# Kernel tuning notes

Hardware: AMD Instinct MI355X
Metric: run time of the kernel (lower is better)

Reference implementation:

```python
import jax, jax.numpy as jnp
import numpy as np

N, NFEAT, NHID, E = 100000, 256, 64, 1600000
EPS = 1e-5
NEG_SLOPE = 0.2


def _glorot(k, shape):
    lim = float(np.sqrt(6.0 / (shape[0] + shape[1])))
    return jax.random.uniform(k, shape, jnp.float32, -lim, lim)


def setup_inputs() -> dict:
    key = jax.random.key(0)
    ks = jax.random.split(key, 24)
    inp = {
        "g": jax.random.normal(ks[0], (N, NFEAT), jnp.float32),           # node features
        "x": jax.random.randint(ks[1], (2, E), 0, N),                      # edge_index [src; dst]
    }
    # estimator GAT params
    inp["est_W"] = _glorot(ks[2], (NFEAT, NHID))
    inp["est_asrc"] = _glorot(ks[3], (NHID, 1))[:, 0]
    inp["est_adst"] = _glorot(ks[4], (NHID, 1))[:, 0]
    inp["est_bias"] = jnp.zeros((NHID,), jnp.float32)
    inp["est_gamma"] = jnp.ones((NHID,), jnp.float32)
    inp["est_beta"] = jnp.zeros((NHID,), jnp.float32)
    inp["est_rmean"] = 0.1 * jax.random.normal(ks[5], (NHID,), jnp.float32)
    inp["est_rvar"] = jax.random.uniform(ks[6], (NHID,), jnp.float32, 0.5, 1.5)
    # GNN GAT params
    inp["gnn_W"] = _glorot(ks[7], (NFEAT, NHID))
    inp["gnn_asrc"] = _glorot(ks[8], (NHID, 1))[:, 0]
    inp["gnn_adst"] = _glorot(ks[9], (NHID, 1))[:, 0]
    inp["gnn_bias"] = jnp.zeros((NHID,), jnp.float32)
    inp["gnn_gamma"] = jnp.ones((NHID,), jnp.float32)
    inp["gnn_beta"] = jnp.zeros((NHID,), jnp.float32)
    inp["gnn_rmean"] = 0.1 * jax.random.normal(ks[10], (NHID,), jnp.float32)
    inp["gnn_rvar"] = jax.random.uniform(ks[11], (NHID,), jnp.float32, 0.5, 1.5)
    # classifier head
    inp["cls_W"] = _glorot(ks[12], (NHID, 1))
    inp["cls_b"] = jnp.zeros((1,), jnp.float32)
    return inp


def _gat(feat, src, dst, W, a_src, a_dst, bias, gamma, beta, rmean, rvar):
    # GATConv (heads=1): linear -> per-edge attention logits -> segment softmax over dst -> weighted scatter
    h = feat @ W                                  # [N, NHID]
    e_src = h @ a_src                             # [N]
    e_dst = h @ a_dst                             # [N]
    e = jax.nn.leaky_relu(e_src[src] + e_dst[dst], NEG_SLOPE)   # [E+N]
    m = jax.ops.segment_max(e, dst, num_segments=N)
    p = jnp.exp(e - m[dst])
    z = jax.ops.segment_sum(p, dst, num_segments=N)
    alpha = p / z[dst]                            # softmax per destination node
    out = jax.ops.segment_sum(h[src] * alpha[:, None], dst, num_segments=N) + bias
    # transition: ReLU -> BatchNorm1d (eval, running stats) -> Dropout (identity in eval)
    out = jnp.maximum(out, 0.0)
    return (out - rmean) * jax.lax.rsqrt(rvar + EPS) * gamma + beta


def reference(g, x, est_W, est_asrc, est_adst, est_bias, est_gamma, est_beta, est_rmean, est_rvar,
              gnn_W, gnn_asrc, gnn_adst, gnn_bias, gnn_gamma, gnn_beta, gnn_rmean, gnn_rvar,
              cls_W, cls_b):
    loop = jnp.arange(N)                          # add_self_loops=True
    src = jnp.concatenate([x[0], loop])
    dst = jnp.concatenate([x[1], loop])
    s = _gat(g, src, dst, est_W, est_asrc, est_adst, est_bias, est_gamma, est_beta, est_rmean, est_rvar)
    z = _gat(g, src, dst, gnn_W, gnn_asrc, gnn_adst, gnn_bias, gnn_gamma, gnn_beta, gnn_rmean, gnn_rvar)
    y = z @ cls_W + cls_b                         # [N, 1]
    return (y, s)
```

## Files before the change

kernel.cpp:

```cpp
#include <hip/hip_runtime.h>
#include <math.h>
#include <float.h>

#define NFEAT 256
#define NHID 64
#define BN_EPS 1e-5f

typedef float f32x4 __attribute__((ext_vector_type(4)));
typedef short s16x8 __attribute__((ext_vector_type(8)));

__device__ __forceinline__ float lrelu(float x) { return x >= 0.f ? x : 0.2f * x; }
__device__ __forceinline__ unsigned short f2bf(float f) {
    unsigned int u = __float_as_uint(f);
    return (unsigned short)((u + 0x7fffu + ((u >> 16) & 1u)) >> 16);
}
__device__ __forceinline__ float bf_lo(unsigned int v) { return __uint_as_float(v << 16); }
__device__ __forceinline__ float bf_hi(unsigned int v) { return __uint_as_float(v & 0xffff0000u); }

__global__ void prep_w_k(const float* __restrict__ We, const float* __restrict__ Wg,
                         unsigned short* __restrict__ Wt, int* __restrict__ bcnt) {
    if (blockIdx.x == 0) bcnt[threadIdx.x] = 0;
    int tid = blockIdx.x * 256 + threadIdx.x;
    int ks  = tid >> 12;
    int col = (tid >> 5) & 127;
    int kk  = tid & 31;
    int k   = ks * 32 + kk;
    float v = (col < 64) ? We[k * 64 + col] : Wg[k * 64 + (col - 64)];
    size_t byte = (size_t)ks * 10240 + col * 80 + (kk >> 3) * 16 + (kk & 7) * 2;
    Wt[byte >> 1] = f2bf(v);
}

__global__ void bucket_hist_k(const int* __restrict__ x, int E, int* __restrict__ bcnt) {
    __shared__ int lh[256];
    int tid = threadIdx.x;
    lh[tid] = 0;
    __syncthreads();
    int base = (blockIdx.x * 256 + tid) * 32;
#pragma unroll
    for (int c = 0; c < 8; ++c) {
        int b4 = base + c * 4;
        if (b4 + 4 <= E) {
            int4 d = *(const int4*)(x + E + b4);
            atomicAdd(&lh[d.x >> 9], 1); atomicAdd(&lh[d.y >> 9], 1);
            atomicAdd(&lh[d.z >> 9], 1); atomicAdd(&lh[d.w >> 9], 1);
        } else {
            for (int k = 0; k < 4; ++k)
                if (b4 + k < E) atomicAdd(&lh[x[E + b4 + k] >> 9], 1);
        }
    }
    __syncthreads();
    if (lh[tid] > 0) atomicAdd(&bcnt[tid], lh[tid]);
}

__global__ void bucket_scan_k(const int* __restrict__ bcnt, int M, int NBKT,
                              int* __restrict__ bucket_base, int* __restrict__ bcursor,
                              int* __restrict__ csr_base) {
    __shared__ int s_c[2][256], s_t[2][256];
    int tid = threadIdx.x;
    int c = (tid < NBKT) ? bcnt[tid] : 0;
    int n0 = tid << 9;
    int sc = (tid < NBKT) ? min(512, M - n0) : 0;
    int tot = c + sc;
    s_c[0][tid] = c; s_t[0][tid] = tot;
    __syncthreads();
    int cur = 0;
    for (int off = 1; off < 256; off <<= 1) {
        int nc = s_c[cur][tid] + (tid >= off ? s_c[cur][tid - off] : 0);
        int nt = s_t[cur][tid] + (tid >= off ? s_t[cur][tid - off] : 0);
        s_c[cur ^ 1][tid] = nc; s_t[cur ^ 1][tid] = nt;
        __syncthreads();
        cur ^= 1;
    }
    if (tid < NBKT) {
        int eb = s_c[cur][tid] - c;
        bucket_base[tid] = eb;
        bcursor[tid] = eb;
        csr_base[tid] = s_t[cur][tid] - tot;
    }
}

__global__ void bucket_scatter_k(const int* __restrict__ x, int E,
                                 int* __restrict__ bcursor, int* __restrict__ ebuf) {
    __shared__ int lh[256], gb[256];
    int tid = threadIdx.x;
    lh[tid] = 0;
    __syncthreads();
    int base = (blockIdx.x * 256 + tid) * 32;
#pragma unroll
    for (int c = 0; c < 8; ++c) {
        int b4 = base + c * 4;
        if (b4 + 4 <= E) {
            int4 d = *(const int4*)(x + E + b4);
            atomicAdd(&lh[d.x >> 9], 1); atomicAdd(&lh[d.y >> 9], 1);
            atomicAdd(&lh[d.z >> 9], 1); atomicAdd(&lh[d.w >> 9], 1);
        } else {
            for (int k = 0; k < 4; ++k)
                if (b4 + k < E) atomicAdd(&lh[x[E + b4 + k] >> 9], 1);
        }
    }
    __syncthreads();
    if (lh[tid] > 0) gb[tid] = atomicAdd(&bcursor[tid], lh[tid]);
    lh[tid] = 0;
    __syncthreads();
#pragma unroll
    for (int c = 0; c < 8; ++c) {
        int b4 = base + c * 4;
        if (b4 + 4 <= E) {
            int4 s = *(const int4*)(x + b4);
            int4 d = *(const int4*)(x + E + b4);
            int ss[4] = {s.x, s.y, s.z, s.w};
            int dd[4] = {d.x, d.y, d.z, d.w};
#pragma unroll
            for (int k = 0; k < 4; ++k) {
                int bk = dd[k] >> 9;
                int rk = atomicAdd(&lh[bk], 1);
                ebuf[gb[bk] + rk] = ((dd[k] & 511) << 17) | ss[k];
            }
        } else {
            for (int k = 0; k < 4; ++k) {
                int i = b4 + k;
                if (i < E) {
                    int sv = x[i], dv = x[E + i];
                    int bk = dv >> 9;
                    int rk = atomicAdd(&lh[bk], 1);
                    ebuf[gb[bk] + rk] = ((dv & 511) << 17) | sv;
                }
            }
        }
    }
}

__global__ __launch_bounds__(256) void bucket_csr_k(const int* __restrict__ bcnt,
                                                    const int* __restrict__ bucket_base,
                                                    const int* __restrict__ csr_base,
                                                    const int* __restrict__ ebuf, int M,
                                                    int* __restrict__ row_start,
                                                    int* __restrict__ deg,
                                                    int* __restrict__ srcs) {
    int b = blockIdx.x, tid = threadIdx.x;
    int nE = bcnt[b];
    int ebase = bucket_base[b];
    int cbase = csr_base[b];
    int n0 = b << 9;
    int nloc = min(512, M - n0);
    __shared__ int cnt[512], sa[512], sb[512], cur[512];
#pragma unroll
    for (int k = 0; k < 2; ++k) {
        int i = tid + k * 256;
        cnt[i] = (i < nloc) ? 1 : 0;
    }
    __syncthreads();
    for (int j = tid; j < nE; j += 256)
        atomicAdd(&cnt[ebuf[ebase + j] >> 17], 1);
    __syncthreads();
#pragma unroll
    for (int k = 0; k < 2; ++k) { int i = tid + k * 256; sa[i] = cnt[i]; }
    __syncthreads();
    int* a = sa; int* bb = sb;
    for (int off = 1; off < 512; off <<= 1) {
#pragma unroll
        for (int k = 0; k < 2; ++k) {
            int i = tid + k * 256;
            bb[i] = a[i] + (i >= off ? a[i - off] : 0);
        }
        __syncthreads();
        int* t = a; a = bb; bb = t;
    }
#pragma unroll
    for (int k = 0; k < 2; ++k) {
        int i = tid + k * 256;
        int excl = a[i] - cnt[i];
        cur[i] = excl;
        if (i < nloc) {
            row_start[n0 + i] = cbase + excl;
            deg[n0 + i] = cnt[i];
            srcs[cbase + excl] = n0 + i;
            cur[i] = excl + 1;
        }
    }
    __syncthreads();
    for (int j = tid; j < nE; j += 256) {
        int p = ebuf[ebase + j];
        int dl = p >> 17, src = p & 0x1FFFF;
        int pos = atomicAdd(&cur[dl], 1);
        srcs[cbase + pos] = src;
    }
}

__global__ __launch_bounds__(256) void gemm_mfma_k(const float* __restrict__ g,
                                                   const char* __restrict__ Wt,
                                                   unsigned short* __restrict__ hh,
                                                   const float* __restrict__ ase,
                                                   const float* __restrict__ ade,
                                                   const float* __restrict__ asg,
                                                   const float* __restrict__ adg,
                                                   float2* __restrict__ esrc,
                                                   float2* __restrict__ edst, int M) {
    __shared__ __align__(16) char lds[21504];
    char* As = lds;
    char* Bs = lds + 10240;
    float* av = (float*)(lds + 20480);
    const int tid = threadIdx.x;
    const int l = tid & 63;
    const int w = tid >> 6;
    const int row0 = blockIdx.x * 128;

    {
        float v;
        if (tid < 64)       v = ase[tid];
        else if (tid < 128) v = ade[tid - 64];
        else if (tid < 192) v = asg[tid - 128];
        else                v = adg[tid - 192];
        av[tid] = v;
    }

    f32x4 acc[2][8];
#pragma unroll
    for (int r = 0; r < 2; r++)
#pragma unroll
        for (int n = 0; n < 8; n++) acc[r][n] = (f32x4){0.f, 0.f, 0.f, 0.f};

    const int arow = tid >> 1;
    const int ah = tid & 1;
    const int grow = row0 + arow;
    const float* gp = g + (size_t)grow * NFEAT + ah * 16;
    const char* wp = Wt + arow * 80 + ah * 32;

    float4 v0 = make_float4(0.f, 0.f, 0.f, 0.f), v1 = v0, v2 = v0, v3 = v0;
    s16x8 b0, b1;
    if (grow < M) {
        v0 = *(const float4*)(gp + 0);
        v1 = *(const float4*)(gp + 4);
        v2 = *(const float4*)(gp + 8);
        v3 = *(const float4*)(gp + 12);
    }
    b0 = *(const s16x8*)(wp);
    b1 = *(const s16x8*)(wp + 16);

    for (int ks = 0; ks < 8; ++ks) {
        {
            s16x8 c0, c1;
            c0[0]=f2bf(v0.x); c0[1]=f2bf(v0.y); c0[2]=f2bf(v0.z); c0[3]=f2bf(v0.w);
            c0[4]=f2bf(v1.x); c0[5]=f2bf(v1.y); c0[6]=f2bf(v1.z); c0[7]=f2bf(v1.w);
            c1[0]=f2bf(v2.x); c1[1]=f2bf(v2.y); c1[2]=f2bf(v2.z); c1[3]=f2bf(v2.w);
            c1[4]=f2bf(v3.x); c1[5]=f2bf(v3.y); c1[6]=f2bf(v3.z); c1[7]=f2bf(v3.w);
            *(s16x8*)(As + arow * 80 + ah * 32)      = c0;
            *(s16x8*)(As + arow * 80 + ah * 32 + 16) = c1;
            *(s16x8*)(Bs + arow * 80 + ah * 32)      = b0;
            *(s16x8*)(Bs + arow * 80 + ah * 32 + 16) = b1;
        }
        __syncthreads();
        if (ks < 7) {
            const float* gpn = gp + (ks + 1) * 32;
            const char* wpn = wp + (size_t)(ks + 1) * 10240;
            v0 = make_float4(0.f, 0.f, 0.f, 0.f); v1 = v0; v2 = v0; v3 = v0;
            if (grow < M) {
                v0 = *(const float4*)(gpn + 0);
                v1 = *(const float4*)(gpn + 4);
                v2 = *(const float4*)(gpn + 8);
                v3 = *(const float4*)(gpn + 12);
            }
            b0 = *(const s16x8*)(wpn);
            b1 = *(const s16x8*)(wpn + 16);
        }
        s16x8 af[2];
#pragma unroll
        for (int r = 0; r < 2; r++)
            af[r] = *(const s16x8*)(As + (w * 32 + r * 16 + (l & 15)) * 80 + (l >> 4) * 16);
#pragma unroll
        for (int n = 0; n < 8; n++) {
            s16x8 bf = *(const s16x8*)(Bs + (n * 16 + (l & 15)) * 80 + (l >> 4) * 16);
            acc[0][n] = __builtin_amdgcn_mfma_f32_16x16x32_bf16(af[0], bf, acc[0][n], 0, 0, 0);
            acc[1][n] = __builtin_amdgcn_mfma_f32_16x16x32_bf16(af[1], bf, acc[1][n], 0, 0, 0);
        }
        __syncthreads();
    }

    float vs_e[4], vd_e[4], vs_g[4], vd_g[4];
    {
        const int l16 = l & 15;
#pragma unroll
        for (int n = 0; n < 4; ++n) {
            vs_e[n] = av[n * 16 + l16];
            vd_e[n] = av[64 + n * 16 + l16];
            vs_g[n] = av[128 + n * 16 + l16];
            vd_g[n] = av[192 + n * 16 + l16];
        }
    }

    unsigned short* epi = (unsigned short*)lds;
#pragma unroll
    for (int p = 0; p < 2; ++p) {
        {
            float pse[4] = {0,0,0,0}, pde[4] = {0,0,0,0};
            float psg[4] = {0,0,0,0}, pdg[4] = {0,0,0,0};
#pragma unroll
            for (int n = 0; n < 4; ++n)
#pragma unroll
                for (int j = 0; j < 4; ++j) {
                    float he = acc[p][n][j];
                    float hg = acc[p][n + 4][j];
                    pse[j] += he * vs_e[n];
                    pde[j] += he * vd_e[n];
                    psg[j] += hg * vs_g[n];
                    pdg[j] += hg * vd_g[n];
                }
#pragma unroll
            for (int off = 1; off <= 8; off <<= 1) {
#pragma unroll
                for (int j = 0; j < 4; ++j) {
                    pse[j] += __shfl_xor(pse[j], off, 64);
                    pde[j] += __shfl_xor(pde[j], off, 64);
                    psg[j] += __shfl_xor(psg[j], off, 64);
                    pdg[j] += __shfl_xor(pdg[j], off, 64);
                }
            }
            if ((l & 15) == 0) {
#pragma unroll
                for (int j = 0; j < 4; ++j) {
                    int gr = row0 + w * 32 + p * 16 + (l >> 4) * 4 + j;
                    if (gr < M) {
                        esrc[gr] = make_float2(pse[j], psg[j]);
                        edst[gr] = make_float2(pde[j], pdg[j]);
                    }
                }
            }
        }
#pragma unroll
        for (int n = 0; n < 8; n++)
#pragma unroll
            for (int j = 0; j < 4; j++)
                epi[(w * 16 + (l >> 4) * 4 + j) * 128 + n * 16 + (l & 15)] = f2bf(acc[p][n][j]);
        __syncthreads();
        int er = tid >> 2, sgm = tid & 3;
        int grow2 = row0 + 32 * (er >> 4) + 16 * p + (er & 15);
        if (grow2 < M) {
            const s16x8* src = (const s16x8*)(epi + er * 128 + sgm * 32);
            s16x8* dst = (s16x8*)(hh + (size_t)grow2 * 128 + sgm * 32);
#pragma unroll
            for (int q = 0; q < 4; q++) dst[q] = src[q];
        }
        __syncthreads();
    }
}

__global__ void node_acc_k(const int* __restrict__ srcs, const int* __restrict__ row_start,
                           const int* __restrict__ deg,
                           const float2* __restrict__ esrc, const float2* __restrict__ edst,
                           const unsigned short* __restrict__ hh,
                           const float* __restrict__ be, const float* __restrict__ ge,
                           const float* __restrict__ bte, const float* __restrict__ rme,
                           const float* __restrict__ rve,
                           const float* __restrict__ bg, const float* __restrict__ gg,
                           const float* __restrict__ btg, const float* __restrict__ rmg,
                           const float* __restrict__ rvg,
                           const float* __restrict__ clsW, const float* __restrict__ clsb,
                           float* __restrict__ y, float* __restrict__ s_out, int M) {
    int n = blockIdx.x * 4 + (threadIdx.x >> 6);
    int l = threadIdx.x & 63;
    if (n >= M) return;
    int beg = row_start[n];
    int cnt = deg[n];
    int qh = l >> 4;
    int li = l & 15;
    int layer = li >> 3;
    float2 ed = edst[n];
    float edv = layer ? ed.y : ed.x;
    const int* sp = srcs + beg;
    const char* hb = (const char*)hh + (unsigned)li * 16;
    float a0 = 0.f, a1 = 0.f, a2 = 0.f, a3 = 0.f;
    float a4 = 0.f, a5 = 0.f, a6 = 0.f, a7 = 0.f, zacc = 0.f;
    int j = 0;
    for (; j + 16 <= cnt; j += 16) {
        int s0 = sp[j + qh];
        int s1 = sp[j + 4 + qh];
        int s2 = sp[j + 8 + qh];
        int s3 = sp[j + 12 + qh];
        float2 e0 = esrc[s0], e1 = esrc[s1], e2 = esrc[s2], e3 = esrc[s3];
        uint4 h0 = *(const uint4*)(hb + ((size_t)(unsigned)s0 << 8));
        uint4 h1 = *(const uint4*)(hb + ((size_t)(unsigned)s1 << 8));
        uint4 h2 = *(const uint4*)(hb + ((size_t)(unsigned)s2 << 8));
        uint4 h3 = *(const uint4*)(hb + ((size_t)(unsigned)s3 << 8));
        float p0 = __expf(lrelu((layer ? e0.y : e0.x) + edv));
        float p1 = __expf(lrelu((layer ? e1.y : e1.x) + edv));
        float p2 = __expf(lrelu((layer ? e2.y : e2.x) + edv));
        float p3 = __expf(lrelu((layer ? e3.y : e3.x) + edv));
        zacc += (p0 + p1) + (p2 + p3);
        a0 += p0 * bf_lo(h0.x); a1 += p0 * bf_hi(h0.x);
        a2 += p0 * bf_lo(h0.y); a3 += p0 * bf_hi(h0.y);
        a4 += p0 * bf_lo(h0.z); a5 += p0 * bf_hi(h0.z);
        a6 += p0 * bf_lo(h0.w); a7 += p0 * bf_hi(h0.w);
        a0 += p1 * bf_lo(h1.x); a1 += p1 * bf_hi(h1.x);
        a2 += p1 * bf_lo(h1.y); a3 += p1 * bf_hi(h1.y);
        a4 += p1 * bf_lo(h1.z); a5 += p1 * bf_hi(h1.z);
        a6 += p1 * bf_lo(h1.w); a7 += p1 * bf_hi(h1.w);
// ... 67 lines not shown
        o0 = (fmaxf(o0 + bA.x, 0.f) - rmA.x) * rsqrtf(rvA.x + BN_EPS) * gA.x + btA.x;
        o1 = (fmaxf(o1 + bA.y, 0.f) - rmA.y) * rsqrtf(rvA.y + BN_EPS) * gA.y + btA.y;
        o2 = (fmaxf(o2 + bA.z, 0.f) - rmA.z) * rsqrtf(rvA.z + BN_EPS) * gA.z + btA.z;
        o3 = (fmaxf(o3 + bA.w, 0.f) - rmA.w) * rsqrtf(rvA.w + BN_EPS) * gA.w + btA.w;
        o4 = (fmaxf(o4 + bB.x, 0.f) - rmB.x) * rsqrtf(rvB.x + BN_EPS) * gB.x + btB.x;
        o5 = (fmaxf(o5 + bB.y, 0.f) - rmB.y) * rsqrtf(rvB.y + BN_EPS) * gB.y + btB.y;
        o6 = (fmaxf(o6 + bB.z, 0.f) - rmB.z) * rsqrtf(rvB.z + BN_EPS) * gB.z + btB.z;
        o7 = (fmaxf(o7 + bB.w, 0.f) - rmB.w) * rsqrtf(rvB.w + BN_EPS) * gB.w + btB.w;
        if (layer == 0) {
            float4* so = (float4*)(s_out + (size_t)n * 64 + (li & 7) * 8);
            so[0] = make_float4(o0, o1, o2, o3);
            so[1] = make_float4(o4, o5, o6, o7);
        } else {
            float4 wA = ((const float4*)clsW)[cb];
            float4 wB = ((const float4*)clsW)[cb + 1];
            float t = o0 * wA.x + o1 * wA.y + o2 * wA.z + o3 * wA.w
                    + o4 * wB.x + o5 * wB.y + o6 * wB.z + o7 * wB.w;
            t += __shfl_xor(t, 1, 64);
            t += __shfl_xor(t, 2, 64);
            t += __shfl_xor(t, 4, 64);
            if (li == 8) y[n] = t + clsb[0];
        }
    }
}

extern "C" void kernel_launch(void* const* d_in, const int* in_sizes, int n_in,
                              void* d_out, int out_size, void* d_ws, size_t ws_size,
                              hipStream_t stream) {
    const float* g        = (const float*)d_in[0];
    const int*   x        = (const int*)d_in[1];
    const float* est_W    = (const float*)d_in[2];
    const float* est_asrc = (const float*)d_in[3];
    const float* est_adst = (const float*)d_in[4];
    const float* est_bias = (const float*)d_in[5];
    const float* est_gamma= (const float*)d_in[6];
    const float* est_beta = (const float*)d_in[7];
    const float* est_rmean= (const float*)d_in[8];
    const float* est_rvar = (const float*)d_in[9];
    const float* gnn_W    = (const float*)d_in[10];
    const float* gnn_asrc = (const float*)d_in[11];
    const float* gnn_adst = (const float*)d_in[12];
    const float* gnn_bias = (const float*)d_in[13];
    const float* gnn_gamma= (const float*)d_in[14];
    const float* gnn_beta = (const float*)d_in[15];
    const float* gnn_rmean= (const float*)d_in[16];
    const float* gnn_rvar = (const float*)d_in[17];
    const float* cls_W    = (const float*)d_in[18];
    const float* cls_b    = (const float*)d_in[19];

    const int M  = in_sizes[0] / NFEAT;
    const int E  = in_sizes[1] / 2;
    const int Et = E + M;
    const int NBKT = (M + 511) >> 9;

    float* y_out = (float*)d_out;
    float* s_out = y_out + M;

    char* base = (char*)d_ws;
    unsigned short* hh = (unsigned short*)base;
    size_t off = (size_t)M * 128 * 2;
    char* Wt = base + off;                  off += 81920;
    float2* esrc = (float2*)(base + off);   off += (size_t)M * 8;
    float2* edst = (float2*)(base + off);   off += (size_t)M * 8;
    int* deg       = (int*)(base + off);    off += (size_t)M * 4;
    int* row_start = (int*)(base + off);    off += (size_t)M * 4;
    int* srcs      = (int*)(base + off);    off += (size_t)Et * 4;
    int* ebuf      = (int*)(base + off);    off += (size_t)E * 4;
    int* bcnt        = (int*)(base + off);  off += 256 * 4;
    int* bucket_base = (int*)(base + off);  off += 256 * 4;
    int* bcursor     = (int*)(base + off);  off += 256 * 4;
    int* csr_base    = (int*)(base + off);  off += 256 * 4;

    const int EB32 = (E + 8191) / 8192;

    prep_w_k<<<128, 256, 0, stream>>>(est_W, gnn_W, (unsigned short*)Wt, bcnt);
    bucket_hist_k<<<EB32, 256, 0, stream>>>(x, E, bcnt);
    bucket_scan_k<<<1, 256, 0, stream>>>(bcnt, M, NBKT, bucket_base, bcursor, csr_base);
    bucket_scatter_k<<<EB32, 256, 0, stream>>>(x, E, bcursor, ebuf);
    bucket_csr_k<<<NBKT, 256, 0, stream>>>(bcnt, bucket_base, csr_base, ebuf, M,
                                           row_start, deg, srcs);

    gemm_mfma_k<<<(M + 127) / 128, 256, 0, stream>>>(g, Wt, hh,
                                                     est_asrc, est_adst, gnn_asrc, gnn_adst,
                                                     esrc, edst, M);

    node_acc_k<<<(M + 3) / 4, 256, 0, stream>>>(srcs, row_start, deg, esrc, edst, hh,
                                                est_bias, est_gamma, est_beta, est_rmean, est_rvar,
                                                gnn_bias, gnn_gamma, gnn_beta, gnn_rmean, gnn_rvar,
                                                cls_W, cls_b, y_out, s_out, M);
}
```

Measured before the change: 175.3 us.

## Merge preprocessing kernels and co-schedule edge scatter with GEMM blocks

Folds the weight conversion into the histogram kernel. Per-block bucket counts are written out and prefix-scanned in a single block, which makes scatter offsets deterministic and removes the global cursor atomics and the second histogram pass inside the scatter. The edge scatter blocks are then appended to the GEMM grid, so the bucketing work overlaps with the MFMA projection and the launch count drops from seven to five. The cost is a serial per-thread loop over all edge blocks in the single-block scan (about 196 iterations), plus LDS usage shared between two very different block types.

```diff
diff --git a/kernel.cpp b/kernel.cpp
--- a/kernel.cpp
+++ b/kernel.cpp
@@ -17,25 +17,27 @@
 __device__ __forceinline__ float bf_lo(unsigned int v) { return __uint_as_float(v << 16); }
 __device__ __forceinline__ float bf_hi(unsigned int v) { return __uint_as_float(v & 0xffff0000u); }
 
-__global__ void prep_w_k(const float* __restrict__ We, const float* __restrict__ Wg,
-                         unsigned short* __restrict__ Wt, int* __restrict__ bcnt) {
-    if (blockIdx.x == 0) bcnt[threadIdx.x] = 0;
-    int tid = blockIdx.x * 256 + threadIdx.x;
-    int ks  = tid >> 12;
-    int col = (tid >> 5) & 127;
-    int kk  = tid & 31;
-    int k   = ks * 32 + kk;
-    float v = (col < 64) ? We[k * 64 + col] : Wg[k * 64 + (col - 64)];
-    size_t byte = (size_t)ks * 10240 + col * 80 + (kk >> 3) * 16 + (kk & 7) * 2;
-    Wt[byte >> 1] = f2bf(v);
-}
-
-__global__ void bucket_hist_k(const int* __restrict__ x, int E, int* __restrict__ bcnt) {
+__global__ void stage1_k(const float* __restrict__ We, const float* __restrict__ Wg,
+                         unsigned short* __restrict__ Wt,
+                         const int* __restrict__ x, int E,
+                         int* __restrict__ blkcnt) {
+    if (blockIdx.x < 128) {
+        int tid = blockIdx.x * 256 + threadIdx.x;
+        int ks  = tid >> 12;
+        int col = (tid >> 5) & 127;
+        int kk  = tid & 31;
+        int k   = ks * 32 + kk;
+        float v = (col < 64) ? We[k * 64 + col] : Wg[k * 64 + (col - 64)];
+        size_t byte = (size_t)ks * 10240 + col * 80 + (kk >> 3) * 16 + (kk & 7) * 2;
+        Wt[byte >> 1] = f2bf(v);
+        return;
+    }
     __shared__ int lh[256];
+    int blk = blockIdx.x - 128;
     int tid = threadIdx.x;
     lh[tid] = 0;
     __syncthreads();
-    int base = (blockIdx.x * 256 + tid) * 32;
+    int base = (blk * 256 + tid) * 32;
 #pragma unroll
     for (int c = 0; c < 8; ++c) {
         int b4 = base + c * 4;
@@ -49,59 +51,53 @@
         }
     }
     __syncthreads();
-    if (lh[tid] > 0) atomicAdd(&bcnt[tid], lh[tid]);
-}
-
-__global__ void bucket_scan_k(const int* __restrict__ bcnt, int M, int NBKT,
-                              int* __restrict__ bucket_base, int* __restrict__ bcursor,
-                              int* __restrict__ csr_base) {
+    blkcnt[blk * 256 + tid] = lh[tid];
+}
+
+__global__ void scan_k(int* __restrict__ blkcnt, int NEB, int M, int NBKT,
+                       int* __restrict__ blkbase,
+                       int* __restrict__ bcnt, int* __restrict__ bucket_base,
+                       int* __restrict__ csr_base) {
     __shared__ int s_c[2][256], s_t[2][256];
-    int tid = threadIdx.x;
-    int c = (tid < NBKT) ? bcnt[tid] : 0;
-    int n0 = tid << 9;
-    int sc = (tid < NBKT) ? min(512, M - n0) : 0;
-    int tot = c + sc;
-    s_c[0][tid] = c; s_t[0][tid] = tot;
+    int t = threadIdx.x;
+    int run = 0;
+    for (int b = 0; b < NEB; ++b) {
+        int c = blkcnt[b * 256 + t];
+        blkbase[b * 256 + t] = run;
+        run += c;
+    }
+    bcnt[t] = run;
+    int n0 = t << 9;
+    int sc = (t < NBKT) ? min(512, M - n0) : 0;
+    int cc = (t < NBKT) ? run : 0;
+    int tot = cc + sc;
+    s_c[0][t] = cc; s_t[0][t] = tot;
     __syncthreads();
     int cur = 0;
     for (int off = 1; off < 256; off <<= 1) {
-        int nc = s_c[cur][tid] + (tid >= off ? s_c[cur][tid - off] : 0);
-        int nt = s_t[cur][tid] + (tid >= off ? s_t[cur][tid - off] : 0);
-        s_c[cur ^ 1][tid] = nc; s_t[cur ^ 1][tid] = nt;
+        int nc = s_c[cur][t] + (t >= off ? s_c[cur][t - off] : 0);
+        int nt = s_t[cur][t] + (t >= off ? s_t[cur][t - off] : 0);
+        s_c[cur ^ 1][t] = nc; s_t[cur ^ 1][t] = nt;
         __syncthreads();
         cur ^= 1;
     }
-    if (tid < NBKT) {
-        int eb = s_c[cur][tid] - c;
-        bucket_base[tid] = eb;
-        bcursor[tid] = eb;
-        csr_base[tid] = s_t[cur][tid] - tot;
-    }
-}
-
-__global__ void bucket_scatter_k(const int* __restrict__ x, int E,
-                                 int* __restrict__ bcursor, int* __restrict__ ebuf) {
-    __shared__ int lh[256], gb[256];
+    int bb = 0;
+    if (t < NBKT) {
+        bb = s_c[cur][t] - cc;
+        bucket_base[t] = bb;
+        csr_base[t] = s_t[cur][t] - tot;
+    }
+    for (int b = 0; b < NEB; ++b)
+        blkbase[b * 256 + t] += bb;
+}
+
+__device__ void scatter_body(const int* __restrict__ x, int E, int blk,
+                             const int* __restrict__ blkbase, int* __restrict__ ebuf) {
+    __shared__ int lh[256];
     int tid = threadIdx.x;
-    lh[tid] = 0;
-    __syncthreads();
-    int base = (blockIdx.x * 256 + tid) * 32;
-#pragma unroll
-    for (int c = 0; c < 8; ++c) {
-        int b4 = base + c * 4;
-        if (b4 + 4 <= E) {
-            int4 d = *(const int4*)(x + E + b4);
-            atomicAdd(&lh[d.x >> 9], 1); atomicAdd(&lh[d.y >> 9], 1);
-            atomicAdd(&lh[d.z >> 9], 1); atomicAdd(&lh[d.w >> 9], 1);
-        } else {
-            for (int k = 0; k < 4; ++k)
-                if (b4 + k < E) atomicAdd(&lh[x[E + b4 + k] >> 9], 1);
-        }
-    }
-    __syncthreads();
-    if (lh[tid] > 0) gb[tid] = atomicAdd(&bcursor[tid], lh[tid]);
-    lh[tid] = 0;
-    __syncthreads();
+    lh[tid] = blkbase[blk * 256 + tid];
+    __syncthreads();
+    int base = (blk * 256 + tid) * 32;
 #pragma unroll
     for (int c = 0; c < 8; ++c) {
         int b4 = base + c * 4;
@@ -113,8 +109,8 @@
 #pragma unroll
             for (int k = 0; k < 4; ++k) {
                 int bk = dd[k] >> 9;
-                int rk = atomicAdd(&lh[bk], 1);
-                ebuf[gb[bk] + rk] = ((dd[k] & 511) << 17) | ss[k];
+                int pos = atomicAdd(&lh[bk], 1);
+                ebuf[pos] = ((dd[k] & 511) << 17) | ss[k];
             }
         } else {
             for (int k = 0; k < 4; ++k) {
@@ -122,11 +118,175 @@
                 if (i < E) {
                     int sv = x[i], dv = x[E + i];
                     int bk = dv >> 9;
-                    int rk = atomicAdd(&lh[bk], 1);
-                    ebuf[gb[bk] + rk] = ((dv & 511) << 17) | sv;
+                    int pos = atomicAdd(&lh[bk], 1);
+                    ebuf[pos] = ((dv & 511) << 17) | sv;
                 }
             }
         }
+    }
+}
+
+__global__ __launch_bounds__(256) void stage3_k(const float* __restrict__ g,
+                                                const char* __restrict__ Wt,
+                                                unsigned short* __restrict__ hh,
+                                                const float* __restrict__ ase,
+                                                const float* __restrict__ ade,
+                                                const float* __restrict__ asg,
+                                                const float* __restrict__ adg,
+                                                float2* __restrict__ esrc,
+                                                float2* __restrict__ edst, int M, int GB,
+                                                const int* __restrict__ x, int E,
+                                                const int* __restrict__ blkbase,
+                                                int* __restrict__ ebuf) {
+    __shared__ __align__(16) char lds[21504];
+    if (blockIdx.x >= (unsigned)GB) {
+        scatter_body(x, E, blockIdx.x - GB, blkbase, ebuf);
+        return;
+    }
+    char* As = lds;
+    char* Bs = lds + 10240;
+    float* av = (float*)(lds + 20480);
+    const int tid = threadIdx.x;
+    const int l = tid & 63;
+    const int w = tid >> 6;
+    const int row0 = blockIdx.x * 128;
+
+    {
+        float v;
+        if (tid < 64)       v = ase[tid];
+        else if (tid < 128) v = ade[tid - 64];
+        else if (tid < 192) v = asg[tid - 128];
+        else                v = adg[tid - 192];
+        av[tid] = v;
+    }
+
+    f32x4 acc[2][8];
+#pragma unroll
+    for (int r = 0; r < 2; r++)
+#pragma unroll
+        for (int n = 0; n < 8; n++) acc[r][n] = (f32x4){0.f, 0.f, 0.f, 0.f};
+
+    const int arow = tid >> 1;
+    const int ah = tid & 1;
+    const int grow = row0 + arow;
+    const float* gp = g + (size_t)grow * NFEAT + ah * 16;
+    const char* wp = Wt + arow * 80 + ah * 32;
+
+    float4 v0 = make_float4(0.f, 0.f, 0.f, 0.f), v1 = v0, v2 = v0, v3 = v0;
+    s16x8 b0, b1;
+    if (grow < M) {
+        v0 = *(const float4*)(gp + 0);
+        v1 = *(const float4*)(gp + 4);
+        v2 = *(const float4*)(gp + 8);
+        v3 = *(const float4*)(gp + 12);
+    }
+    b0 = *(const s16x8*)(wp);
+    b1 = *(const s16x8*)(wp + 16);
+
+    for (int ks = 0; ks < 8; ++ks) {
+        {
+            s16x8 c0, c1;
+            c0[0]=f2bf(v0.x); c0[1]=f2bf(v0.y); c0[2]=f2bf(v0.z); c0[3]=f2bf(v0.w);
+            c0[4]=f2bf(v1.x); c0[5]=f2bf(v1.y); c0[6]=f2bf(v1.z); c0[7]=f2bf(v1.w);
+            c1[0]=f2bf(v2.x); c1[1]=f2bf(v2.y); c1[2]=f2bf(v2.z); c1[3]=f2bf(v2.w);
+            c1[4]=f2bf(v3.x); c1[5]=f2bf(v3.y); c1[6]=f2bf(v3.z); c1[7]=f2bf(v3.w);
+            *(s16x8*)(As + arow * 80 + ah * 32)      = c0;
+            *(s16x8*)(As + arow * 80 + ah * 32 + 16) = c1;
+            *(s16x8*)(Bs + arow * 80 + ah * 32)      = b0;
+            *(s16x8*)(Bs + arow * 80 + ah * 32 + 16) = b1;
+        }
+        __syncthreads();
+        if (ks < 7) {
+            const float* gpn = gp + (ks + 1) * 32;
+            const char* wpn = wp + (size_t)(ks + 1) * 10240;
+            v0 = make_float4(0.f, 0.f, 0.f, 0.f); v1 = v0; v2 = v0; v3 = v0;
+            if (grow < M) {
+                v0 = *(const float4*)(gpn + 0);
+                v1 = *(const float4*)(gpn + 4);
+                v2 = *(const float4*)(gpn + 8);
+                v3 = *(const float4*)(gpn + 12);
+            }
+            b0 = *(const s16x8*)(wpn);
+            b1 = *(const s16x8*)(wpn + 16);
+        }
+        s16x8 af[2];
+#pragma unroll
+        for (int r = 0; r < 2; r++)
+            af[r] = *(const s16x8*)(As + (w * 32 + r * 16 + (l & 15)) * 80 + (l >> 4) * 16);
+#pragma unroll
+        for (int n = 0; n < 8; n++) {
+            s16x8 bf = *(const s16x8*)(Bs + (n * 16 + (l & 15)) * 80 + (l >> 4) * 16);
+            acc[0][n] = __builtin_amdgcn_mfma_f32_16x16x32_bf16(af[0], bf, acc[0][n], 0, 0, 0);
+            acc[1][n] = __builtin_amdgcn_mfma_f32_16x16x32_bf16(af[1], bf, acc[1][n], 0, 0, 0);
+        }
+        __syncthreads();
+    }
+
+    float vs_e[4], vd_e[4], vs_g[4], vd_g[4];
+    {
+        const int l16 = l & 15;
+#pragma unroll
+        for (int n = 0; n < 4; ++n) {
+            vs_e[n] = av[n * 16 + l16];
+            vd_e[n] = av[64 + n * 16 + l16];
+            vs_g[n] = av[128 + n * 16 + l16];
+            vd_g[n] = av[192 + n * 16 + l16];
+        }
+    }
+
+    unsigned short* epi = (unsigned short*)lds;
+#pragma unroll
+    for (int p = 0; p < 2; ++p) {
+        {
+            float pse[4] = {0,0,0,0}, pde[4] = {0,0,0,0};
+            float psg[4] = {0,0,0,0}, pdg[4] = {0,0,0,0};
+#pragma unroll
+            for (int n = 0; n < 4; ++n)
+#pragma unroll
+                for (int j = 0; j < 4; ++j) {
+                    float he = acc[p][n][j];
+                    float hg = acc[p][n + 4][j];
+                    pse[j] += he * vs_e[n];
+                    pde[j] += he * vd_e[n];
+                    psg[j] += hg * vs_g[n];
+                    pdg[j] += hg * vd_g[n];
+                }
+#pragma unroll
+            for (int off = 1; off <= 8; off <<= 1) {
+#pragma unroll
+                for (int j = 0; j < 4; ++j) {
+                    pse[j] += __shfl_xor(pse[j], off, 64);
+                    pde[j] += __shfl_xor(pde[j], off, 64);
+                    psg[j] += __shfl_xor(psg[j], off, 64);
+                    pdg[j] += __shfl_xor(pdg[j], off, 64);
+                }
+            }
+            if ((l & 15) == 0) {
+#pragma unroll
+                for (int j = 0; j < 4; ++j) {
+                    int gr = row0 + w * 32 + p * 16 + (l >> 4) * 4 + j;
+                    if (gr < M) {
+                        esrc[gr] = make_float2(pse[j], psg[j]);
+                        edst[gr] = make_float2(pde[j], pdg[j]);
+                    }
+                }
+            }
+        }
+#pragma unroll
+        for (int n = 0; n < 8; n++)
+#pragma unroll
+            for (int j = 0; j < 4; j++)
+                epi[(w * 16 + (l >> 4) * 4 + j) * 128 + n * 16 + (l & 15)] = f2bf(acc[p][n][j]);
+        __syncthreads();
+        int er = tid >> 2, sgm = tid & 3;
+        int grow2 = row0 + 32 * (er >> 4) + 16 * p + (er & 15);
+        if (grow2 < M) {
+            const s16x8* src = (const s16x8*)(epi + er * 128 + sgm * 32);
+            s16x8* dst = (s16x8*)(hh + (size_t)grow2 * 128 + sgm * 32);
+#pragma unroll
+            for (int q = 0; q < 4; q++) dst[q] = src[q];
+        }
+        __syncthreads();
     }
 }
 
@@ -184,163 +344,6 @@
         int dl = p >> 17, src = p & 0x1FFFF;
         int pos = atomicAdd(&cur[dl], 1);
         srcs[cbase + pos] = src;
-    }
-}
-
-__global__ __launch_bounds__(256) void gemm_mfma_k(const float* __restrict__ g,
-                                                   const char* __restrict__ Wt,
-                                                   unsigned short* __restrict__ hh,
-                                                   const float* __restrict__ ase,
-                                                   const float* __restrict__ ade,
-                                                   const float* __restrict__ asg,
-                                                   const float* __restrict__ adg,
-                                                   float2* __restrict__ esrc,
-                                                   float2* __restrict__ edst, int M) {
-    __shared__ __align__(16) char lds[21504];
-    char* As = lds;
-    char* Bs = lds + 10240;
-    float* av = (float*)(lds + 20480);
-    const int tid = threadIdx.x;
-    const int l = tid & 63;
-    const int w = tid >> 6;
-    const int row0 = blockIdx.x * 128;
-
-    {
-        float v;
-        if (tid < 64)       v = ase[tid];
-        else if (tid < 128) v = ade[tid - 64];
-        else if (tid < 192) v = asg[tid - 128];
-        else                v = adg[tid - 192];
-        av[tid] = v;
-    }
-
-    f32x4 acc[2][8];
-#pragma unroll
-    for (int r = 0; r < 2; r++)
-#pragma unroll
-        for (int n = 0; n < 8; n++) acc[r][n] = (f32x4){0.f, 0.f, 0.f, 0.f};
-
-    const int arow = tid >> 1;
-    const int ah = tid & 1;
-    const int grow = row0 + arow;
-    const float* gp = g + (size_t)grow * NFEAT + ah * 16;
-    const char* wp = Wt + arow * 80 + ah * 32;
-
-    float4 v0 = make_float4(0.f, 0.f, 0.f, 0.f), v1 = v0, v2 = v0, v3 = v0;
-    s16x8 b0, b1;
-    if (grow < M) {
-        v0 = *(const float4*)(gp + 0);
-        v1 = *(const float4*)(gp + 4);
-        v2 = *(const float4*)(gp + 8);
-        v3 = *(const float4*)(gp + 12);
-    }
-    b0 = *(const s16x8*)(wp);
-    b1 = *(const s16x8*)(wp + 16);
-
-    for (int ks = 0; ks < 8; ++ks) {
-        {
-            s16x8 c0, c1;
-            c0[0]=f2bf(v0.x); c0[1]=f2bf(v0.y); c0[2]=f2bf(v0.z); c0[3]=f2bf(v0.w);
-            c0[4]=f2bf(v1.x); c0[5]=f2bf(v1.y); c0[6]=f2bf(v1.z); c0[7]=f2bf(v1.w);
-            c1[0]=f2bf(v2.x); c1[1]=f2bf(v2.y); c1[2]=f2bf(v2.z); c1[3]=f2bf(v2.w);
-            c1[4]=f2bf(v3.x); c1[5]=f2bf(v3.y); c1[6]=f2bf(v3.z); c1[7]=f2bf(v3.w);
-            *(s16x8*)(As + arow * 80 + ah * 32)      = c0;
-            *(s16x8*)(As + arow * 80 + ah * 32 + 16) = c1;
-            *(s16x8*)(Bs + arow * 80 + ah * 32)      = b0;
-            *(s16x8*)(Bs + arow * 80 + ah * 32 + 16) = b1;
-        }
-        __syncthreads();
-        if (ks < 7) {
-            const float* gpn = gp + (ks + 1) * 32;
-            const char* wpn = wp + (size_t)(ks + 1) * 10240;
-            v0 = make_float4(0.f, 0.f, 0.f, 0.f); v1 = v0; v2 = v0; v3 = v0;
-            if (grow < M) {
-                v0 = *(const float4*)(gpn + 0);
-                v1 = *(const float4*)(gpn + 4);
-                v2 = *(const float4*)(gpn + 8);
-                v3 = *(const float4*)(gpn + 12);
-            }
-            b0 = *(const s16x8*)(wpn);
-            b1 = *(const s16x8*)(wpn + 16);
-        }
-        s16x8 af[2];
-#pragma unroll
-        for (int r = 0; r < 2; r++)
-            af[r] = *(const s16x8*)(As + (w * 32 + r * 16 + (l & 15)) * 80 + (l >> 4) * 16);
-#pragma unroll
-        for (int n = 0; n < 8; n++) {
-            s16x8 bf = *(const s16x8*)(Bs + (n * 16 + (l & 15)) * 80 + (l >> 4) * 16);
-            acc[0][n] = __builtin_amdgcn_mfma_f32_16x16x32_bf16(af[0], bf, acc[0][n], 0, 0, 0);
-            acc[1][n] = __builtin_amdgcn_mfma_f32_16x16x32_bf16(af[1], bf, acc[1][n], 0, 0, 0);
-        }
-        __syncthreads();
-    }
-
-    float vs_e[4], vd_e[4], vs_g[4], vd_g[4];
-    {
-        const int l16 = l & 15;
-#pragma unroll
-        for (int n = 0; n < 4; ++n) {
-            vs_e[n] = av[n * 16 + l16];
-            vd_e[n] = av[64 + n * 16 + l16];
-            vs_g[n] = av[128 + n * 16 + l16];
-            vd_g[n] = av[192 + n * 16 + l16];
-        }
-    }
-
-    unsigned short* epi = (unsigned short*)lds;
-#pragma unroll
-    for (int p = 0; p < 2; ++p) {
-        {
-            float pse[4] = {0,0,0,0}, pde[4] = {0,0,0,0};
-            float psg[4] = {0,0,0,0}, pdg[4] = {0,0,0,0};
-#pragma unroll
-            for (int n = 0; n < 4; ++n)
-#pragma unroll
-                for (int j = 0; j < 4; ++j) {
-                    float he = acc[p][n][j];
-                    float hg = acc[p][n + 4][j];
-                    pse[j] += he * vs_e[n];
-                    pde[j] += he * vd_e[n];
-                    psg[j] += hg * vs_g[n];
-                    pdg[j] += hg * vd_g[n];
-                }
-#pragma unroll
-            for (int off = 1; off <= 8; off <<= 1) {
-#pragma unroll
-                for (int j = 0; j < 4; ++j) {
-                    pse[j] += __shfl_xor(pse[j], off, 64);
-                    pde[j] += __shfl_xor(pde[j], off, 64);
-                    psg[j] += __shfl_xor(psg[j], off, 64);
-                    pdg[j] += __shfl_xor(pdg[j], off, 64);
-                }
-            }
-            if ((l & 15) == 0) {
-#pragma unroll
-                for (int j = 0; j < 4; ++j) {
-                    int gr = row0 + w * 32 + p * 16 + (l >> 4) * 4 + j;
-                    if (gr < M) {
-                        esrc[gr] = make_float2(pse[j], psg[j]);
-                        edst[gr] = make_float2(pde[j], pdg[j]);
-                    }
-                }
-            }
-        }
-#pragma unroll
-        for (int n = 0; n < 8; n++)
-#pragma unroll
-            for (int j = 0; j < 4; j++)
-                epi[(w * 16 + (l >> 4) * 4 + j) * 128 + n * 16 + (l & 15)] = f2bf(acc[p][n][j]);
-        __syncthreads();
-        int er = tid >> 2, sgm = tid & 3;
-        int grow2 = row0 + 32 * (er >> 4) + 16 * p + (er & 15);
-        if (grow2 < M) {
-            const s16x8* src = (const s16x8*)(epi + er * 128 + sgm * 32);
-            s16x8* dst = (s16x8*)(hh + (size_t)grow2 * 128 + sgm * 32);
-#pragma unroll
-            for (int q = 0; q < 4; q++) dst[q] = src[q];
-        }
-        __syncthreads();
     }
 }
 
@@ -514,6 +517,8 @@
     const int E  = in_sizes[1] / 2;
     const int Et = E + M;
     const int NBKT = (M + 511) >> 9;
+    const int NEB  = (E + 8191) / 8192;
+    const int GB   = (M + 127) / 128;
 
     float* y_out = (float*)d_out;
     float* s_out = y_out + M;
@@ -528,24 +533,21 @@
     int* row_start = (int*)(base + off);    off += (size_t)M * 4;
     int* srcs      = (int*)(base + off);    off += (size_t)Et * 4;
     int* ebuf      = (int*)(base + off);    off += (size_t)E * 4;
+    int* blkcnt    = (int*)(base + off);    off += (size_t)NEB * 256 * 4;
+    int* blkbase   = (int*)(base + off);    off += (size_t)NEB * 256 * 4;
     int* bcnt        = (int*)(base + off);  off += 256 * 4;
     int* bucket_base = (int*)(base + off);  off += 256 * 4;
-    int* bcursor     = (int*)(base + off);  off += 256 * 4;
     int* csr_base    = (int*)(base + off);  off += 256 * 4;
 
-    const int EB32 = (E + 8191) / 8192;
-
-    prep_w_k<<<128, 256, 0, stream>>>(est_W, gnn_W, (unsigned short*)Wt, bcnt);
-    bucket_hist_k<<<EB32, 256, 0, stream>>>(x, E, bcnt);
-    bucket_scan_k<<<1, 256, 0, stream>>>(bcnt, M, NBKT, bucket_base, bcursor, csr_base);
-    bucket_scatter_k<<<EB32, 256, 0, stream>>>(x, E, bcursor, ebuf);
+    stage1_k<<<128 + NEB, 256, 0, stream>>>(est_W, gnn_W, (unsigned short*)Wt,
+                                            x, E, blkcnt);
+    scan_k<<<1, 256, 0, stream>>>(blkcnt, NEB, M, NBKT, blkbase,
+                                  bcnt, bucket_base, csr_base);
+    stage3_k<<<GB + NEB, 256, 0, stream>>>(g, Wt, hh,
+                                           est_asrc, est_adst, gnn_asrc, gnn_adst,
+                                           esrc, edst, M, GB, x, E, blkbase, ebuf);
     bucket_csr_k<<<NBKT, 256, 0, stream>>>(bcnt, bucket_base, csr_base, ebuf, M,
                                            row_start, deg, srcs);
-
-    gemm_mfma_k<<<(M + 127) / 128, 256, 0, stream>>>(g, Wt, hh,
-                                                     est_asrc, est_adst, gnn_asrc, gnn_adst,
-                                                     esrc, edst, M);
-
     node_acc_k<<<(M + 3) / 4, 256, 0, stream>>>(srcs, row_start, deg, esrc, edst, hh,
                                                 est_bias, est_gamma, est_beta, est_rmean, est_rvar,
                                                 gnn_bias, gnn_gamma, gnn_beta, gnn_rmean, gnn_rvar,
```

After: 234.7 us. +33.9%, slower.

## Fuse edge bucket scatter and MFMA GEMM into one heterogeneous launch

Applied to the files above, without the earlier changes.

Merges the bucket scatter kernel and the bf16 MFMA projection GEMM into a single kernel whose first GB blocks run the GEMM and the remaining blocks run the edge scatter. The two stages are independent, so this removes one launch and lets the memory-bound scatter overlap with the GEMM instead of running serially. The scatter blocks now reserve the GEMM's larger LDS footprint, which may lower their occupancy.

```diff
diff --git a/kernel.cpp b/kernel.cpp
--- a/kernel.cpp
+++ b/kernel.cpp
@@ -79,13 +79,13 @@
     }
 }
 
-__global__ void bucket_scatter_k(const int* __restrict__ x, int E,
-                                 int* __restrict__ bcursor, int* __restrict__ ebuf) {
-    __shared__ int lh[256], gb[256];
+__device__ void scatter_body(const int* __restrict__ x, int E, int blk,
+                             int* __restrict__ bcursor, int* __restrict__ ebuf,
+                             int* lh, int* gb) {
     int tid = threadIdx.x;
     lh[tid] = 0;
     __syncthreads();
-    int base = (blockIdx.x * 256 + tid) * 32;
+    int base = (blk * 256 + tid) * 32;
 #pragma unroll
     for (int c = 0; c < 8; ++c) {
         int b4 = base + c * 4;
@@ -130,6 +130,171 @@
     }
 }
 
+__global__ __launch_bounds__(256) void stage3_k(const float* __restrict__ g,
+                                                const char* __restrict__ Wt,
+                                                unsigned short* __restrict__ hh,
+                                                const float* __restrict__ ase,
+                                                const float* __restrict__ ade,
+                                                const float* __restrict__ asg,
+                                                const float* __restrict__ adg,
+                                                float2* __restrict__ esrc,
+                                                float2* __restrict__ edst, int M, int GB,
+                                                const int* __restrict__ x, int E,
+                                                int* __restrict__ bcursor,
+                                                int* __restrict__ ebuf) {
+    __shared__ __align__(16) char lds[21504];
+    __shared__ int sc_lh[256], sc_gb[256];
+    if (blockIdx.x >= (unsigned)GB) {
+        scatter_body(x, E, blockIdx.x - GB, bcursor, ebuf, sc_lh, sc_gb);
+        return;
+    }
+    char* As = lds;
+    char* Bs = lds + 10240;
+    float* av = (float*)(lds + 20480);
+    const int tid = threadIdx.x;
+    const int l = tid & 63;
+    const int w = tid >> 6;
+    const int row0 = blockIdx.x * 128;
+
+    {
+        float v;
+        if (tid < 64)       v = ase[tid];
+        else if (tid < 128) v = ade[tid - 64];
+        else if (tid < 192) v = asg[tid - 128];
+        else                v = adg[tid - 192];
+        av[tid] = v;
+    }
+
+    f32x4 acc[2][8];
+#pragma unroll
+    for (int r = 0; r < 2; r++)
+#pragma unroll
+        for (int n = 0; n < 8; n++) acc[r][n] = (f32x4){0.f, 0.f, 0.f, 0.f};
+
+    const int arow = tid >> 1;
+    const int ah = tid & 1;
+    const int grow = row0 + arow;
+    const float* gp = g + (size_t)grow * NFEAT + ah * 16;
+    const char* wp = Wt + arow * 80 + ah * 32;
+
+    float4 v0 = make_float4(0.f, 0.f, 0.f, 0.f), v1 = v0, v2 = v0, v3 = v0;
+    s16x8 b0, b1;
+    if (grow < M) {
+        v0 = *(const float4*)(gp + 0);
+        v1 = *(const float4*)(gp + 4);
+        v2 = *(const float4*)(gp + 8);
+        v3 = *(const float4*)(gp + 12);
+    }
+    b0 = *(const s16x8*)(wp);
+    b1 = *(const s16x8*)(wp + 16);
+
+    for (int ks = 0; ks < 8; ++ks) {
+        {
+            s16x8 c0, c1;
+            c0[0]=f2bf(v0.x); c0[1]=f2bf(v0.y); c0[2]=f2bf(v0.z); c0[3]=f2bf(v0.w);
+            c0[4]=f2bf(v1.x); c0[5]=f2bf(v1.y); c0[6]=f2bf(v1.z); c0[7]=f2bf(v1.w);
+            c1[0]=f2bf(v2.x); c1[1]=f2bf(v2.y); c1[2]=f2bf(v2.z); c1[3]=f2bf(v2.w);
+            c1[4]=f2bf(v3.x); c1[5]=f2bf(v3.y); c1[6]=f2bf(v3.z); c1[7]=f2bf(v3.w);
+            *(s16x8*)(As + arow * 80 + ah * 32)      = c0;
+            *(s16x8*)(As + arow * 80 + ah * 32 + 16) = c1;
+            *(s16x8*)(Bs + arow * 80 + ah * 32)      = b0;
+            *(s16x8*)(Bs + arow * 80 + ah * 32 + 16) = b1;
+        }
+        __syncthreads();
+        if (ks < 7) {
+            const float* gpn = gp + (ks + 1) * 32;
+            const char* wpn = wp + (size_t)(ks + 1) * 10240;
+            v0 = make_float4(0.f, 0.f, 0.f, 0.f); v1 = v0; v2 = v0; v3 = v0;
+            if (grow < M) {
+                v0 = *(const float4*)(gpn + 0);
+                v1 = *(const float4*)(gpn + 4);
+                v2 = *(const float4*)(gpn + 8);
+                v3 = *(const float4*)(gpn + 12);
+            }
+            b0 = *(const s16x8*)(wpn);
+            b1 = *(const s16x8*)(wpn + 16);
+        }
+        s16x8 af[2];
+#pragma unroll
+        for (int r = 0; r < 2; r++)
+            af[r] = *(const s16x8*)(As + (w * 32 + r * 16 + (l & 15)) * 80 + (l >> 4) * 16);
+#pragma unroll
+        for (int n = 0; n < 8; n++) {
+            s16x8 bf = *(const s16x8*)(Bs + (n * 16 + (l & 15)) * 80 + (l >> 4) * 16);
+            acc[0][n] = __builtin_amdgcn_mfma_f32_16x16x32_bf16(af[0], bf, acc[0][n], 0, 0, 0);
+            acc[1][n] = __builtin_amdgcn_mfma_f32_16x16x32_bf16(af[1], bf, acc[1][n], 0, 0, 0);
+        }
+        __syncthreads();
+    }
+
+    float vs_e[4], vd_e[4], vs_g[4], vd_g[4];
+    {
+        const int l16 = l & 15;
+#pragma unroll
+        for (int n = 0; n < 4; ++n) {
+            vs_e[n] = av[n * 16 + l16];
+            vd_e[n] = av[64 + n * 16 + l16];
+            vs_g[n] = av[128 + n * 16 + l16];
+            vd_g[n] = av[192 + n * 16 + l16];
+        }
+    }
+
+    unsigned short* epi = (unsigned short*)lds;
+#pragma unroll
+    for (int p = 0; p < 2; ++p) {
+        {
+            float pse[4] = {0,0,0,0}, pde[4] = {0,0,0,0};
+            float psg[4] = {0,0,0,0}, pdg[4] = {0,0,0,0};
+#pragma unroll
+            for (int n = 0; n < 4; ++n)
+#pragma unroll
+                for (int j = 0; j < 4; ++j) {
+                    float he = acc[p][n][j];
+                    float hg = acc[p][n + 4][j];
+                    pse[j] += he * vs_e[n];
+                    pde[j] += he * vd_e[n];
+                    psg[j] += hg * vs_g[n];
+                    pdg[j] += hg * vd_g[n];
+                }
+#pragma unroll
+            for (int off = 1; off <= 8; off <<= 1) {
+#pragma unroll
+                for (int j = 0; j < 4; ++j) {
+                    pse[j] += __shfl_xor(pse[j], off, 64);
+                    pde[j] += __shfl_xor(pde[j], off, 64);
+                    psg[j] += __shfl_xor(psg[j], off, 64);
+                    pdg[j] += __shfl_xor(pdg[j], off, 64);
+                }
+            }
+            if ((l & 15) == 0) {
+#pragma unroll
+                for (int j = 0; j < 4; ++j) {
+                    int gr = row0 + w * 32 + p * 16 + (l >> 4) * 4 + j;
+                    if (gr < M) {
+                        esrc[gr] = make_float2(pse[j], psg[j]);
+                        edst[gr] = make_float2(pde[j], pdg[j]);
+                    }
+                }
+            }
+        }
+#pragma unroll
+        for (int n = 0; n < 8; n++)
+#pragma unroll
+            for (int j = 0; j < 4; j++)
+                epi[(w * 16 + (l >> 4) * 4 + j) * 128 + n * 16 + (l & 15)] = f2bf(acc[p][n][j]);
+        __syncthreads();
+        int er = tid >> 2, sgm = tid & 3;
+        int grow2 = row0 + 32 * (er >> 4) + 16 * p + (er & 15);
+        if (grow2 < M) {
+            const s16x8* src = (const s16x8*)(epi + er * 128 + sgm * 32);
+            s16x8* dst = (s16x8*)(hh + (size_t)grow2 * 128 + sgm * 32);
+#pragma unroll
+            for (int q = 0; q < 4; q++) dst[q] = src[q];
+        }
+        __syncthreads();
+    }
+}
+
 __global__ __launch_bounds__(256) void bucket_csr_k(const int* __restrict__ bcnt,
                                                     const int* __restrict__ bucket_base,
                                                     const int* __restrict__ csr_base,
@@ -184,163 +349,6 @@
         int dl = p >> 17, src = p & 0x1FFFF;
         int pos = atomicAdd(&cur[dl], 1);
         srcs[cbase + pos] = src;
-    }
-}
-
-__global__ __launch_bounds__(256) void gemm_mfma_k(const float* __restrict__ g,
-                                                   const char* __restrict__ Wt,
-                                                   unsigned short* __restrict__ hh,
-                                                   const float* __restrict__ ase,
-                                                   const float* __restrict__ ade,
-                                                   const float* __restrict__ asg,
-                                                   const float* __restrict__ adg,
-                                                   float2* __restrict__ esrc,
-                                                   float2* __restrict__ edst, int M) {
-    __shared__ __align__(16) char lds[21504];
-    char* As = lds;
-    char* Bs = lds + 10240;
-    float* av = (float*)(lds + 20480);
-    const int tid = threadIdx.x;
-    const int l = tid & 63;
-    const int w = tid >> 6;
-    const int row0 = blockIdx.x * 128;
-
-    {
-        float v;
-        if (tid < 64)       v = ase[tid];
-        else if (tid < 128) v = ade[tid - 64];
-        else if (tid < 192) v = asg[tid - 128];
-        else                v = adg[tid - 192];
-        av[tid] = v;
-    }
-
-    f32x4 acc[2][8];
-#pragma unroll
-    for (int r = 0; r < 2; r++)
-#pragma unroll
-        for (int n = 0; n < 8; n++) acc[r][n] = (f32x4){0.f, 0.f, 0.f, 0.f};
-
-    const int arow = tid >> 1;
-    const int ah = tid & 1;
-    const int grow = row0 + arow;
-    const float* gp = g + (size_t)grow * NFEAT + ah * 16;
-    const char* wp = Wt + arow * 80 + ah * 32;
-
-    float4 v0 = make_float4(0.f, 0.f, 0.f, 0.f), v1 = v0, v2 = v0, v3 = v0;
-    s16x8 b0, b1;
-    if (grow < M) {
-        v0 = *(const float4*)(gp + 0);
-        v1 = *(const float4*)(gp + 4);
-        v2 = *(const float4*)(gp + 8);
-        v3 = *(const float4*)(gp + 12);
-    }
-    b0 = *(const s16x8*)(wp);
-    b1 = *(const s16x8*)(wp + 16);
-
-    for (int ks = 0; ks < 8; ++ks) {
-        {
-            s16x8 c0, c1;
-            c0[0]=f2bf(v0.x); c0[1]=f2bf(v0.y); c0[2]=f2bf(v0.z); c0[3]=f2bf(v0.w);
-            c0[4]=f2bf(v1.x); c0[5]=f2bf(v1.y); c0[6]=f2bf(v1.z); c0[7]=f2bf(v1.w);
-            c1[0]=f2bf(v2.x); c1[1]=f2bf(v2.y); c1[2]=f2bf(v2.z); c1[3]=f2bf(v2.w);
-            c1[4]=f2bf(v3.x); c1[5]=f2bf(v3.y); c1[6]=f2bf(v3.z); c1[7]=f2bf(v3.w);
-            *(s16x8*)(As + arow * 80 + ah * 32)      = c0;
-            *(s16x8*)(As + arow * 80 + ah * 32 + 16) = c1;
-            *(s16x8*)(Bs + arow * 80 + ah * 32)      = b0;
-            *(s16x8*)(Bs + arow * 80 + ah * 32 + 16) = b1;
-        }
-        __syncthreads();
-        if (ks < 7) {
-            const float* gpn = gp + (ks + 1) * 32;
-            const char* wpn = wp + (size_t)(ks + 1) * 10240;
-            v0 = make_float4(0.f, 0.f, 0.f, 0.f); v1 = v0; v2 = v0; v3 = v0;
-            if (grow < M) {
-                v0 = *(const float4*)(gpn + 0);
-                v1 = *(const float4*)(gpn + 4);
-                v2 = *(const float4*)(gpn + 8);
-                v3 = *(const float4*)(gpn + 12);
-            }
-            b0 = *(const s16x8*)(wpn);
-            b1 = *(const s16x8*)(wpn + 16);
-        }
-        s16x8 af[2];
-#pragma unroll
-        for (int r = 0; r < 2; r++)
-            af[r] = *(const s16x8*)(As + (w * 32 + r * 16 + (l & 15)) * 80 + (l >> 4) * 16);
-#pragma unroll
-        for (int n = 0; n < 8; n++) {
-            s16x8 bf = *(const s16x8*)(Bs + (n * 16 + (l & 15)) * 80 + (l >> 4) * 16);
-            acc[0][n] = __builtin_amdgcn_mfma_f32_16x16x32_bf16(af[0], bf, acc[0][n], 0, 0, 0);
-            acc[1][n] = __builtin_amdgcn_mfma_f32_16x16x32_bf16(af[1], bf, acc[1][n], 0, 0, 0);
-        }
-        __syncthreads();
-    }
-
-    float vs_e[4], vd_e[4], vs_g[4], vd_g[4];
-    {
-        const int l16 = l & 15;
-#pragma unroll
-        for (int n = 0; n < 4; ++n) {
-            vs_e[n] = av[n * 16 + l16];
-            vd_e[n] = av[64 + n * 16 + l16];
-            vs_g[n] = av[128 + n * 16 + l16];
-            vd_g[n] = av[192 + n * 16 + l16];
-        }
-    }
-
-    unsigned short* epi = (unsigned short*)lds;
-#pragma unroll
-    for (int p = 0; p < 2; ++p) {
-        {
-            float pse[4] = {0,0,0,0}, pde[4] = {0,0,0,0};
-            float psg[4] = {0,0,0,0}, pdg[4] = {0,0,0,0};
-#pragma unroll
-            for (int n = 0; n < 4; ++n)
-#pragma unroll
-                for (int j = 0; j < 4; ++j) {
-                    float he = acc[p][n][j];
-                    float hg = acc[p][n + 4][j];
-                    pse[j] += he * vs_e[n];
-                    pde[j] += he * vd_e[n];
-                    psg[j] += hg * vs_g[n];
-                    pdg[j] += hg * vd_g[n];
-                }
-#pragma unroll
-            for (int off = 1; off <= 8; off <<= 1) {
-#pragma unroll
-                for (int j = 0; j < 4; ++j) {
-                    pse[j] += __shfl_xor(pse[j], off, 64);
-                    pde[j] += __shfl_xor(pde[j], off, 64);
-                    psg[j] += __shfl_xor(psg[j], off, 64);
-                    pdg[j] += __shfl_xor(pdg[j], off, 64);
-                }
-            }
-            if ((l & 15) == 0) {
-#pragma unroll
-                for (int j = 0; j < 4; ++j) {
-                    int gr = row0 + w * 32 + p * 16 + (l >> 4) * 4 + j;
-                    if (gr < M) {
-                        esrc[gr] = make_float2(pse[j], psg[j]);
-                        edst[gr] = make_float2(pde[j], pdg[j]);
-                    }
-                }
-            }
-        }
-#pragma unroll
-        for (int n = 0; n < 8; n++)
-#pragma unroll
-            for (int j = 0; j < 4; j++)
-                epi[(w * 16 + (l >> 4) * 4 + j) * 128 + n * 16 + (l & 15)] = f2bf(acc[p][n][j]);
-        __syncthreads();
-        int er = tid >> 2, sgm = tid & 3;
-        int grow2 = row0 + 32 * (er >> 4) + 16 * p + (er & 15);
-        if (grow2 < M) {
-            const s16x8* src = (const s16x8*)(epi + er * 128 + sgm * 32);
-            s16x8* dst = (s16x8*)(hh + (size_t)grow2 * 128 + sgm * 32);
-#pragma unroll
-            for (int q = 0; q < 4; q++) dst[q] = src[q];
-        }
-        __syncthreads();
     }
 }
 
@@ -514,6 +522,8 @@
     const int E  = in_sizes[1] / 2;
     const int Et = E + M;
     const int NBKT = (M + 511) >> 9;
+    const int NEB  = (E + 8191) / 8192;
+    const int GB   = (M + 127) / 128;
 
     float* y_out = (float*)d_out;
     float* s_out = y_out + M;
@@ -533,19 +543,14 @@
     int* bcursor     = (int*)(base + off);  off += 256 * 4;
     int* csr_base    = (int*)(base + off);  off += 256 * 4;
 
-    const int EB32 = (E + 8191) / 8192;
-
     prep_w_k<<<128, 256, 0, stream>>>(est_W, gnn_W, (unsigned short*)Wt, bcnt);
-    bucket_hist_k<<<EB32, 256, 0, stream>>>(x, E, bcnt);
+    bucket_hist_k<<<NEB, 256, 0, stream>>>(x, E, bcnt);
     bucket_scan_k<<<1, 256, 0, stream>>>(bcnt, M, NBKT, bucket_base, bcursor, csr_base);
-    bucket_scatter_k<<<EB32, 256, 0, stream>>>(x, E, bcursor, ebuf);
+    stage3_k<<<GB + NEB, 256, 0, stream>>>(g, Wt, hh,
+                                           est_asrc, est_adst, gnn_asrc, gnn_adst,
+                                           esrc, edst, M, GB, x, E, bcursor, ebuf);
     bucket_csr_k<<<NBKT, 256, 0, stream>>>(bcnt, bucket_base, csr_base, ebuf, M,
                                            row_start, deg, srcs);
-
-    gemm_mfma_k<<<(M + 127) / 128, 256, 0, stream>>>(g, Wt, hh,
-                                                     est_asrc, est_adst, gnn_asrc, gnn_adst,
-                                                     esrc, edst, M);
-
     node_acc_k<<<(M + 3) / 4, 256, 0, stream>>>(srcs, row_start, deg, esrc, edst, hh,
                                                 est_bias, est_gamma, est_beta, est_rmean, est_rvar,
                                                 gnn_bias, gnn_gamma, gnn_beta, gnn_rmean, gnn_rvar,
```

Result: faster. 168.2 us (-4.1%).
